# Optimization experiments

Hardware: AMD Instinct MI355X
Metric: run time of the kernel (lower is better)

## Reference

```python
import jax, jax.numpy as jnp
import numpy as np

D, P, MC = 512, 256, 128   # state dim, obs dim, control dim
H, M, T = 32, 64, 1024     # num filters, Hankel/filter length, horizon
GAMMA = 0.9


def setup_inputs() -> dict:
    rng = np.random.default_rng(0)
    # Stable dynamics: scale spectral radius to 0.95
    A = rng.standard_normal((D, D)).astype(np.float32)
    A *= np.float32(0.95 / np.max(np.abs(np.linalg.eigvals(A))))
    B = (rng.standard_normal((D, MC)) / np.sqrt(D)).astype(np.float32)
    C = (rng.standard_normal((P, D)) / np.sqrt(D)).astype(np.float32)
    # SPD cost matrices
    Q_obs = np.eye(P, dtype=np.float32)
    R = (0.1 * np.eye(MC)).astype(np.float32)
    # LQR-like feedback gain (small, applied to y_obs as in the source)
    K = (0.02 * rng.standard_normal((MC, P))).astype(np.float32)
    # Spectral filters from Hankel matrix: Z_ij = gamma^(i+j+2) * 2/((i+j+2)^3-(i+j+2))
    idx = np.arange(M)
    ij = idx[:, None] + idx[None, :] + 2
    Z = (GAMMA ** ij) * 2.0 / (ij ** 3 - ij)
    w, V = np.linalg.eigh(Z)
    sigma = np.abs(w[-H:])
    phi = V[:, -H:]
    sigma_phi = (sigma ** 0.25)[:, None] * phi.T        # [H, M]
    sigma_phi_M = sigma_phi.astype(np.float32)
    # sum over the inner l-loop of sigma_phi_m (the source sums contributions over l)
    s_m = sigma_phi.sum(axis=1).astype(np.float32)       # [H]
    # Learned controller tensor M_il -> [m_control, H, h, p]
    M_tensor = (0.01 * rng.standard_normal((MC, H, H, P))).astype(np.float32)
    x0 = rng.standard_normal(D).astype(np.float32)
    return {
        "A": jnp.asarray(A), "B": jnp.asarray(B), "C": jnp.asarray(C),
        "Q_obs": jnp.asarray(Q_obs), "R": jnp.asarray(R), "K": jnp.asarray(K),
        "M_tensor": jnp.asarray(M_tensor),
        "sigma_phi_M": jnp.asarray(sigma_phi_M), "s_m": jnp.asarray(s_m),
        "x0": jnp.asarray(x0),
    }


def reference(A, B, C, Q_obs, R, K, M_tensor, sigma_phi_M, s_m, x0):
    h, m = sigma_phi_M.shape          # filters, history window
    mc = B.shape[1]
    p = C.shape[0]

    # CAB[i] = C @ A^i @ B for i = 0..h  (Markov parameters for y_nat)
    def pow_step(Ap, _):
        return Ap @ A, C @ (Ap @ B)
    _, CAB = jax.lax.scan(pow_step, jnp.eye(A.shape[0], dtype=A.dtype), None, length=h + 1)  # [h+1, p, mc]

    # Pre-contract M_tensor with the inner filter weights (sum over j/l):
    # u_pert[c] = sum_{i,k,p'} M2[c,i,p'] * sigma_phi_M[i,k] * y_nat_{t-k}[p']
    M2 = jnp.einsum('cijq,j->ciq', M_tensor, s_m)  # [mc, h, p]

    def step(carry, _):
        x, u_buf, y_buf = carry            # x:[d], u_buf:[h+1,mc] newest-first, y_buf:[m,p] newest-first
        y_obs = C @ x                      # [p]
        # natural observation: strip effect of past controls
        y_nat = y_obs - jnp.einsum('ipc,ic->p', CAB, u_buf)
        y_buf = jnp.concatenate([y_nat[None, :], y_buf[:-1]], axis=0)
        # spectral projection of y_nat history, then contract with learned tensor
        y_proj = sigma_phi_M @ y_buf       # [h, p]
        u_pert = jnp.einsum('ciq,iq->c', M2, y_proj)  # [mc]
        u = -(K @ y_obs) + u_pert
        cost = y_obs @ (Q_obs @ y_obs) + u @ (R @ u)
        u_buf = jnp.concatenate([u[None, :], u_buf[:-1]], axis=0)
        x = A @ x + B @ u
        return (x, u_buf, y_buf), cost

    init = (x0,
            jnp.zeros((h + 1, mc), dtype=x0.dtype),
            jnp.zeros((m, p), dtype=x0.dtype))
    _, costs = jax.lax.scan(step, init, None, length=T)
    return costs  # [T] per-step losses
```

## Files before the change

### kernel.cpp

```cpp
#include <hip/hip_runtime.h>

#define TPB 256
#define NWG 160
#define MAXJ 48

__device__ __forceinline__ void cst(float* p, float v) {
  __hip_atomic_store(p, v, __ATOMIC_RELAXED, __HIP_MEMORY_SCOPE_AGENT);
}
__device__ __forceinline__ void cstu(unsigned* p, unsigned v) {
  __hip_atomic_store(p, v, __ATOMIC_RELAXED, __HIP_MEMORY_SCOPE_AGENT);
}
__device__ __forceinline__ float cld(const float* p) {
  return __hip_atomic_load(p, __ATOMIC_RELAXED, __HIP_MEMORY_SCOPE_AGENT);
}
__device__ __forceinline__ float2 cld2(const float* p) {
  unsigned long long u = __hip_atomic_load(
      reinterpret_cast<const unsigned long long*>(p), __ATOMIC_RELAXED,
      __HIP_MEMORY_SCOPE_AGENT);
  float2 v;
  __builtin_memcpy(&v, &u, 8);
  return v;
}

__device__ __forceinline__ void grid_barrier(unsigned* __restrict__ arr,
                                             int bid, int tid, unsigned phase) {
  asm volatile("s_waitcnt vmcnt(0)" ::: "memory");
  __syncthreads();
  if (tid == 0)
    __hip_atomic_store(arr + (bid << 5), phase, __ATOMIC_RELAXED,
                       __HIP_MEMORY_SCOPE_AGENT);
  if (tid < NWG) {
    while (__hip_atomic_load(arr + (tid << 5), __ATOMIC_RELAXED,
                             __HIP_MEMORY_SCOPE_AGENT) < phase)
      __builtin_amdgcn_s_sleep(1);
  }
  __atomic_signal_fence(__ATOMIC_SEQ_CST);
// ... 86 lines not shown
}

__global__ __launch_bounds__(256) void wfir_kernel(const float* __restrict__ M2g,
    const float* __restrict__ Phi, float* __restrict__ W) {
  int idx = blockIdx.x * 256 + threadIdx.x;
  if (idx >= 64 * 32768) return;
  int j = idx >> 15;
  int cq = idx & 32767;
  int c = cq >> 8;
  int q = cq & 255;
  float acc = 0.f;
#pragma unroll
  for (int i = 0; i < 32; ++i)
    acc = fmaf(Phi[(i << 6) | j], M2g[(size_t)(((c << 5) | i) << 8) | q], acc);
  W[idx] = acc;
}

__global__ __launch_bounds__(256) void axpy_acl(const float* __restrict__ A,
    const float* __restrict__ BKC, float* __restrict__ Acl, float* __restrict__ P1) {
  int i = blockIdx.x * 256 + threadIdx.x;
  if (i < 262144) {
    float v = A[i] - BKC[i];
    Acl[i] = v;
    P1[i] = v;
  }
}

__global__ void init_kernel(const float* __restrict__ x0, float* __restrict__ xh,
    float* __restrict__ eh, float* __restrict__ ynh, float* __restrict__ uh0,
    float* __restrict__ dbnd, unsigned* __restrict__ arr) {
  int i = blockIdx.x * 256 + threadIdx.x;
  int stride = gridDim.x * 256;
  for (int k = i; k < 524288; k += stride) cst(xh + k, 0.f);
  for (int k = i; k < 139392; k += stride) cst(eh + k, 0.f);
  for (int k = i; k < 262144; k += stride) cst(ynh + k, 0.f);
  for (int k = i; k < 8192; k += stride) cst(uh0 + k, 0.f);
  for (int k = i; k < NWG * 32; k += stride) cstu(arr + k, 0u);
  if (i < 512) cst(dbnd + i, x0[i]);
}

#define SVIDX(i) ((((i) >> 7) * 132) + ((i) & 127))

__device__ __forceinline__ void stagePad(float* dst, const float* src, int tid) {
  float2 v = cld2(src + (tid << 1));
  int i = tid << 1;
  int a = SVIDX(i);
  dst[a] = v.x;
  dst[a + 1] = v.y;
}

__global__ __launch_bounds__(TPB, 1) void main_kernel(
    const float* __restrict__ B, const float* __restrict__ C,
    const float* __restrict__ x0, const float* __restrict__ Wfir,
    const float* __restrict__ KC, const float* __restrict__ W0C,
    const float* __restrict__ Pp, const float* __restrict__ CApp,
    const float* __restrict__ W0CAp, const float* __restrict__ Rnp,
    const float* __restrict__ AB33p, const float* __restrict__ CAB33p,
    const float* __restrict__ W0CAB33p, const float* __restrict__ A16k,
    float* __restrict__ xh, float* __restrict__ uh0, float* __restrict__ eh,
    float* __restrict__ ynh, float* __restrict__ dbnd,
    unsigned* __restrict__ arr) {
  __shared__ float smA[64 * 256];
  __shared__ float smY[16 * 256];
  __shared__ float smV[528];
  __shared__ float smW[16 * 128];
  __shared__ float redsc[4][16];
  const int bid = blockIdx.x;
  const int tid = threadIdx.x;

  if (bid < 128) {
    for (int i = tid; i < 16384; i += TPB) {
      int j = i >> 8;
      smA[i] = (j >= 1) ? Wfir[(size_t)j * 32768 + bid * 256 + (i & 255)] : 0.f;
    }
  }
  __syncthreads();

  unsigned bcnt = 0;
#pragma unroll 1
  for (int ph = 0; ph <= 64; ++ph) {
    const int T = ph * 16;
    const int Tp = T - 16;

    if (bid < 32) {
      if (ph < 64) {
        const int s = bid >> 1;
        const int half = (bid & 1) << 7;
        stagePad(smV, dbnd + (size_t)ph * 512, tid);
        __syncthreads();
        const float* Mrow = (s == 0) ? C : (CApp + (size_t)(s - 1) * 131072);
        const int row = half + (tid >> 1);
        const int q0 = (tid & 1) * 2;
        const float4* m4 = (const float4*)(Mrow + (size_t)row * 512 + (tid & 1) * 256);
        const float4* v0 = (const float4*)(smV + q0 * 132);
        const float4* v1 = (const float4*)(smV + (q0 + 1) * 132);
        float a0 = 0.f, a1 = 0.f;
#pragma unroll
        for (int it = 0; it < 32; ++it) {
          float4 mm = m4[it], vv = v0[it];
          a0 += mm.x * vv.x + mm.y * vv.y + mm.z * vv.z + mm.w * vv.w;
        }
#pragma unroll
        for (int it = 0; it < 32; ++it) {
          float4 mm = m4[32 + it], vv = v1[it];
          a1 += mm.x * vv.x + mm.y * vv.y + mm.z * vv.z + mm.w * vv.w;
        }
        float a = a0 + a1;
        a += __shfl_down(a, 1);
        if ((tid & 1) == 0) atomicAdd(&ynh[(size_t)(T + s) * 256 + row], a);
        __syncthreads();
      }
    } else if (bid < 48) {
      if (ph < 64) {
        const int g = bid - 32;
        for (int i2 = tid; i2 < 1024; i2 += TPB) {
          float2 v = cld2(uh0 + (size_t)(64 + T - 33) * 128 + 2 * i2);
          smW[2 * i2] = v.x;
          smW[2 * i2 + 1] = v.y;
        }
        __syncthreads();
        const int row = g * 16 + (tid >> 4);
        const int l16 = tid & 15;
        const int qs = l16 * 8;
        float acc[16];
#pragma unroll
        for (int s = 0; s < 16; ++s) acc[s] = 0.f;
#pragma unroll
        for (int m = 0; m < 15; ++m) {
          const float4* cr = (const float4*)(CAB33p + (size_t)m * 32768 + (size_t)row * 128 + qs);
          float4 c0 = cr[0], c1 = cr[1];
#pragma unroll
          for (int s = 0; s < 16; ++s) {
            if (s > m) {
              const float* u = smW + (s - m - 1) * 128 + qs;
              acc[s] += c0.x * u[0] + c0.y * u[1] + c0.z * u[2] + c0.w * u[3] +
                        c1.x * u[4] + c1.y * u[5] + c1.z * u[6] + c1.w * u[7];
            }
          }
        }
#pragma unroll
        for (int s = 0; s < 16; ++s) {
          float v = acc[s];
          v += __shfl_xor(v, 8);
          v += __shfl_xor(v, 4);
          v += __shfl_xor(v, 2);
          v += __shfl_xor(v, 1);
          if (l16 == 0 && s >= 1) atomicAdd(&ynh[(size_t)(T + s) * 256 + row], v);
        }
        __syncthreads();
      }
    } else if (bid < 64) {
      if (ph < 64) {
        const int s = bid - 48;
        stagePad(smV, dbnd + (size_t)ph * 512, tid);
        __syncthreads();
        const float* Mrow = (s == 0) ? W0C : (W0CAp + (size_t)(s - 1) * 65536);
        const int row = tid >> 1;
        const int q0 = (tid & 1) * 2;
        const float4* m4 = (const float4*)(Mrow + (size_t)row * 512 + (tid & 1) * 256);
        const float4* v0 = (const float4*)(smV + q0 * 132);
        const float4* v1 = (const float4*)(smV + (q0 + 1) * 132);
        float a0 = 0.f, a1 = 0.f;
#pragma unroll
        for (int it = 0; it < 32; ++it) {
          float4 mm = m4[it], vv = v0[it];
          a0 += mm.x * vv.x + mm.y * vv.y + mm.z * vv.z + mm.w * vv.w;
        }
#pragma unroll
        for (int it = 0; it < 32; ++it) {
          float4 mm = m4[32 + it], vv = v1[it];
          a1 += mm.x * vv.x + mm.y * vv.y + mm.z * vv.z + mm.w * vv.w;
        }
        float a = a0 + a1;
        a += __shfl_down(a, 1);
        if ((tid & 1) == 0) atomicAdd(&eh[(size_t)(T + s) * 128 + row], a);
        __syncthreads();
      }
    } else if (bid < 72) {
      if (ph < 64) {
        const int g = bid - 64;
        for (int i2 = tid; i2 < 1024; i2 += TPB) {
          float2 v = cld2(uh0 + (size_t)(64 + T - 33) * 128 + 2 * i2);
          smW[2 * i2] = v.x;
          smW[2 * i2 + 1] = v.y;
        }
        __syncthreads();
        const int row = g * 16 + (tid >> 4);
        const int l16 = tid & 15;
        const int qs = l16 * 8;
        float acc[16];
#pragma unroll
        for (int s = 0; s < 16; ++s) acc[s] = 0.f;
#pragma unroll
        for (int m = 0; m < 15; ++m) {
          const float4* cr = (const float4*)(W0CAB33p + (size_t)m * 16384 + (size_t)row * 128 + qs);
          float4 c0 = cr[0], c1 = cr[1];
#pragma unroll
          for (int s = 0; s < 16; ++s) {
            if (s > m) {
              const float* u = smW + (s - m - 1) * 128 + qs;
              acc[s] += c0.x * u[0] + c0.y * u[1] + c0.z * u[2] + c0.w * u[3] +
                        c1.x * u[4] + c1.y * u[5] + c1.z * u[6] + c1.w * u[7];
            }
          }
        }
#pragma unroll
        for (int s = 0; s < 16; ++s) {
          float v = acc[s];
          v += __shfl_xor(v, 8);
          v += __shfl_xor(v, 4);
          v += __shfl_xor(v, 2);
          v += __shfl_xor(v, 1);
          if (l16 == 0 && s >= 1) atomicAdd(&eh[(size_t)(T + s) * 128 + row], v);
        }
        __syncthreads();
      }
    } else if (bid < 88) {
      if (ph < 64) {
        const int g = bid - 72;
        stagePad(smV, dbnd + (size_t)ph * 512, tid);
        for (int i2 = tid; i2 < 1024; i2 += TPB) {
          float2 v = cld2(uh0 + (size_t)(64 + T - 33) * 128 + 2 * i2);
          smW[2 * i2] = v.x;
          smW[2 * i2 + 1] = v.y;
        }
        __syncthreads();
        const int row = g * 32 + (tid >> 3);
        const int l8 = tid & 7;
        float a = 0.f;
        {
          const float4* m4 = (const float4*)(A16k + (size_t)row * 512 + l8 * 64);
          const float4* v4 = (const float4*)(smV + (l8 >> 1) * 132 + (l8 & 1) * 64);
#pragma unroll
          for (int it = 0; it < 16; ++it) {
            float4 mm = m4[it], vv = v4[it];
            a += mm.x * vv.x + mm.y * vv.y + mm.z * vv.z + mm.w * vv.w;
          }
        }
#pragma unroll
        for (int m = 0; m < 16; ++m) {
          const float4* m4 = (const float4*)(AB33p + (size_t)m * 65536 + (size_t)row * 128 + l8 * 16);
          const float4* v4 = (const float4*)(smW + (15 - m) * 128 + l8 * 16);
#pragma unroll
          for (int it = 0; it < 4; ++it) {
            float4 mm = m4[it], vv = v4[it];
            a += mm.x * vv.x + mm.y * vv.y + mm.z * vv.z + mm.w * vv.w;
          }
        }
        a += __shfl_down(a, 4);
        a += __shfl_down(a, 2);
        a += __shfl_down(a, 1);
        if (l8 == 0) cst(&dbnd[(size_t)(ph + 1) * 512 + row], a);
        __syncthreads();
      }
    } else if (bid < 120) {
      if (ph >= 1) {
        const int w = bid - 88;
        const int s = w >> 1;
        const int half = (w & 1) << 8;
        {
          const float* src = (ph == 1) ? x0 : (xh + (size_t)(Tp - 1) * 512);
          stagePad(smV, src, tid);
        }
        __syncthreads();
        const int pslot = (ph == 1) ? s : (s + 1);
        const int row = half + tid;
        if (pslot == 0) {
          atomicAdd(&xh[(size_t)(Tp + s) * 512 + row], smV[SVIDX(row)]);
        } else {
          const float* Mrow = Pp + (size_t)(pslot - 1) * 262144 + (size_t)row * 512;
          const float4* m4 = (const float4*)Mrow;
          float a0 = 0.f, a1 = 0.f, a2 = 0.f, a3 = 0.f;
          const float4* vq0 = (const float4*)(smV);
          const float4* vq1 = (const float4*)(smV + 132);
          const float4* vq2 = (const float4*)(smV + 264);
          const float4* vq3 = (const float4*)(smV + 396);
#pragma unroll
          for (int it = 0; it < 32; ++it) {
            float4 mm = m4[it], vv = vq0[it];
            a0 += mm.x * vv.x + mm.y * vv.y + mm.z * vv.z + mm.w * vv.w;
          }
#pragma unroll
          for (int it = 0; it < 32; ++it) {
            float4 mm = m4[32 + it], vv = vq1[it];
            a1 += mm.x * vv.x + mm.y * vv.y + mm.z * vv.z + mm.w * vv.w;
          }
#pragma unroll
          for (int it = 0; it < 32; ++it) {
            float4 mm = m4[64 + it], vv = vq2[it];
            a2 += mm.x * vv.x + mm.y * vv.y + mm.z * vv.z + mm.w * vv.w;
          }
#pragma unroll
          for (int it = 0; it < 32; ++it) {
            float4 mm = m4[96 + it], vv = vq3[it];
            a3 += mm.x * vv.x + mm.y * vv.y + mm.z * vv.z + mm.w * vv.w;
          }
          atomicAdd(&xh[(size_t)(Tp + s) * 512 + row], (a0 + a1) + (a2 + a3));
        }
        __syncthreads();
      }
    } else {
      if (ph >= 1 && bid < 152) {
        const int g = bid - 120;
        for (int i2 = tid; i2 < 1024; i2 += TPB) {
          int idx = 2 * i2;
          int r = idx >> 7;
          float2 v;
          if (ph == 1 && r == 0) {
            v.x = 0.f;
            v.y = 0.f;
          } else {
            v = cld2(eh + (size_t)(Tp - 1 + r) * 128 + (idx & 127));
          }
          smW[idx] = v.x;
          smW[idx + 1] = v.y;
        }
        __syncthreads();
        const int row = g * 16 + (tid >> 4);
        const int l16 = tid & 15;
        const int qs = l16 * 8;
        float acc[16];
#pragma unroll
        for (int s = 0; s < 16; ++s) acc[s] = 0.f;
#pragma unroll
        for (int i = 0; i < 16; ++i) {
          const float* Rrow = (i == 0) ? (B + (size_t)row * 128 + qs)
                                       : (Rnp + (size_t)(i - 1) * 65536 + (size_t)row * 128 + qs);
          const float4* cr = (const float4*)Rrow;
          float4 c0 = cr[0], c1 = cr[1];
#pragma unroll
          for (int s = 0; s < 16; ++s) {
            if (s >= i) {
              const float* e = smW + (s - i) * 128 + qs;
              acc[s] += c0.x * e[0] + c0.y * e[1] + c0.z * e[2] + c0.w * e[3] +
                        c1.x * e[4] + c1.y * e[5] + c1.z * e[6] + c1.w * e[7];
            }
          }
        }
#pragma unroll
        for (int s = 0; s < 16; ++s) {
          float v = acc[s];
          v += __shfl_xor(v, 8);
          v += __shfl_xor(v, 4);
          v += __shfl_xor(v, 2);
          v += __shfl_xor(v, 1);
          if (l16 == 0) atomicAdd(&xh[(size_t)(Tp + s) * 512 + row], v);
        }
        __syncthreads();
      }
    }

    grid_barrier(arr, bid, tid, ++bcnt);

    if (bid < 128) {
      if (ph < 64) {
        const int c = bid;
        for (int i2 = tid; i2 < 2048; i2 += TPB) {
          float2 v = cld2(ynh + (size_t)T * 256 + 2 * i2);
          smY[2 * i2] = v.x;
          smY[2 * i2 + 1] = v.y;
        }
        __syncthreads();
        const int q = tid;
        float yreg[16];
#pragma unroll
        for (int s = 0; s < 16; ++s) yreg[s] = smY[s * 256 + q];
        const int wv = tid >> 6;
        const int lane = tid & 63;
#pragma unroll
        for (int kt = 0; kt < 5; ++kt) {
          const int r0 = 1 + 16 * kt;
          float wreg[31];
#pragma unroll
          for (int i = 0; i < 31; ++i) {
            const int j = r0 - 15 + i;
            wreg[i] = (j >= 1 && j <= 63) ? smA[j * 256 + q] : 0.f;
          }
          float acc[16];
#pragma unroll
          for (int a = 0; a < 16; ++a) acc[a] = 0.f;
#pragma unroll
          for (int a = 0; a < 16; ++a)
#pragma unroll
            for (int s = 0; s < 16; ++s) acc[a] += wreg[a + 15 - s] * yreg[s];
#pragma unroll
          for (int a = 0; a < 16; ++a) {
            float v = acc[a];
            v += __shfl_xor(v, 32);
            v += __shfl_xor(v, 16);
            v += __shfl_xor(v, 8);
            v += __shfl_xor(v, 4);
            v += __shfl_xor(v, 2);
            v += __shfl_xor(v, 1);
            if (lane == 0) redsc[wv][a] = v;
          }
          __syncthreads();
          if (tid < 16) {
            float sum = redsc[0][tid] + redsc[1][tid] + redsc[2][tid] + redsc[3][tid];
            atomicAdd(&eh[(size_t)(T + r0 + tid) * 128 + c], sum);
          }
          __syncthreads();
        }
      }
    } else {
      if (ph >= 1) {
        const int g = bid - 128;
        const int s = g >> 1;
        const int ch = (g & 1) * 64;
        const int t = Tp + s;
        stagePad(smV, xh + (size_t)t * 512, tid);
        __syncthreads();
        const int row = ch + (tid >> 2);
        const int q0 = tid & 3;
        const float4* m4 = (const float4*)(KC + (size_t)row * 512 + q0 * 128);
        const float4* v4 = (const float4*)(smV + q0 * 132);
        float a = 0.f;
#pragma unroll
        for (int it = 0; it < 32; ++it) {
          float4 mm = m4[it], vv = v4[it];
          a += mm.x * vv.x + mm.y * vv.y + mm.z * vv.z + mm.w * vv.w;
        }
        a += __shfl_down(a, 2);
        a += __shfl_down(a, 1);
        if ((tid & 3) == 0) {
          float u = cld(&eh[(size_t)t * 128 + row]) - a;
          cst(&uh0[(size_t)(64 + t) * 128 + row], u);
        }
        __syncthreads();
      }
    }

    grid_barrier(arr, bid, tid, ++bcnt);
  }
}

__global__ __launch_bounds__(256) void cost_kernel(const float* __restrict__ C,
    const float* __restrict__ Q, const float* __restrict__ R,
    const float* __restrict__ xh, const float* __restrict__ uh0,
    float* __restrict__ out) {
  __shared__ float xs[512];
  __shared__ float ys[256];
  __shared__ float us[128];
  __shared__ float redw[4];
  const int t = blockIdx.x;
  const int tid = threadIdx.x;
  {
    float2 v = cld2(xh + (size_t)t * 512 + 2 * tid);
    xs[2 * tid] = v.x;
    xs[2 * tid + 1] = v.y;
  }
  if (tid < 64) {
    float2 v = cld2(uh0 + (size_t)(64 + t) * 128 + 2 * tid);
    us[2 * tid] = v.x;
    us[2 * tid + 1] = v.y;
  }
  __syncthreads();
  {
    const float4* m4 = (const float4*)(C + (size_t)tid * 512);
    const float4* v4 = (const float4*)xs;
    float a = 0.f;
    for (int it = 0; it < 128; ++it) {
      float4 mm = m4[it], vv = v4[it];
      a += mm.x * vv.x + mm.y * vv.y + mm.z * vv.z + mm.w * vv.w;
    }
    ys[tid] = a;
// ... 11 lines not shown
    float ru = 0.f;
    for (int k = 0; k < 128; ++k) ru = fmaf(Rr[k], us[k], ru);
    acc += ru * us[tid];
  }
  float v = acc;
  v += __shfl_xor(v, 32);
  v += __shfl_xor(v, 16);
  v += __shfl_xor(v, 8);
  v += __shfl_xor(v, 4);
  v += __shfl_xor(v, 2);
  v += __shfl_xor(v, 1);
  if ((tid & 63) == 0) redw[tid >> 6] = v;
  __syncthreads();
  if (tid == 0) out[t] = redw[0] + redw[1] + redw[2] + redw[3];
}

extern "C" void kernel_launch(void* const* d_in, const int* in_sizes, int n_in,
                              void* d_out, int out_size, void* d_ws, size_t ws_size,
                              hipStream_t stream) {
  (void)in_sizes; (void)n_in; (void)out_size; (void)ws_size;
  const float* A = (const float*)d_in[0];
  const float* B = (const float*)d_in[1];
  const float* C = (const float*)d_in[2];
  const float* Q = (const float*)d_in[3];
  const float* R = (const float*)d_in[4];
  const float* Km = (const float*)d_in[5];
  const float* MT = (const float*)d_in[6];
  const float* Phi = (const float*)d_in[7];
  const float* sm = (const float*)d_in[8];
  const float* x0 = (const float*)d_in[9];

  float* ws = (float*)d_ws;
  const int oWfir = 0;
  const int oPp = 2097152;
  const int oCApp = 6291456;
  const int oW0CAp = 8388608;
  const int oRnp = 9437184;
  const int oAB33 = 10485760;
  const int oCAB33 = 11599872;
  const int oW0CAB33 = 12156928;
  const int oA16 = 12435456;
  const int oKC = 12697600;
  const int oW0C = 12763136;
  const int oAcl = 12828672;
  const int oM2 = 13090816;
  const int oA2 = oM2, oA4 = oM2 + 262144, oA8 = oM2 + 524288, oA32 = oM2 + 786432;
  const int oApB = 14139392;
  const int oxh = 15187968;
  const int ouh0 = 15712256;
  const int oeh = 15851520;
  const int oynh = 15990912;
  const int odbnd = 16253056;
  const int oarr = 16286336;
  const int oBKC = oAB33;

  float* xh = ws + oxh;
  float* uh0 = ws + ouh0;
  float* eh = ws + oeh;
  float* ynh = ws + oynh;
  float* dbnd = ws + odbnd;
  unsigned* arr = (unsigned*)(ws + oarr);

  JobBatch jb;
  jb.n = 0;
  jb.start[0] = 0;
  auto J = [&](int xs_, int xo, int ys_, int yo, int zo, int M, int N, int K) {
    int i = jb.n++;
    jb.xsel[i] = xs_; jb.xoff[i] = xo; jb.ysel[i] = ys_; jb.yoff[i] = yo;
    jb.zoff[i] = zo; jb.M[i] = M; jb.N[i] = N; jb.K[i] = K;
    jb.start[i + 1] = jb.start[i] + (M >> 6) * (N >> 6);
  };
  auto L = [&]() {
    multi_gemm<<<dim3(jb.start[jb.n]), dim3(256), 0, stream>>>(jb, A, B, C, Km, ws);
    jb.n = 0;
    jb.start[0] = 0;
  };

  m2_kernel<<<dim3(4096), dim3(256), 0, stream>>>(MT, sm, ws + oM2);
  wfir_kernel<<<dim3(8192), dim3(256), 0, stream>>>(ws + oM2, Phi, ws + oWfir);

  J(4, 0, 3, 0, oKC, 128, 512, 256);
  J(1, 0, 1, 0, oA2, 512, 512, 512);
  J(1, 0, 2, 0, oApB, 512, 128, 512);
  J(3, 0, 1, 0, oCApp, 256, 512, 512);
  L();
  J(2, 0, 0, oKC, oBKC, 512, 512, 128);
  J(0, oA2, 0, oA2, oA4, 512, 512, 512);
  J(0, oCApp, 1, 0, oCApp + 131072, 256, 512, 512);
  J(1, 0, 0, oApB, oApB + 65536, 512, 128, 512);
  J(0, oWfir, 3, 0, oW0C, 128, 512, 256);
  L();
  axpy_acl<<<dim3(1024), dim3(256), 0, stream>>>(A, ws + oBKC, ws + oAcl, ws + oPp);
  J(0, oA4, 0, oA4, oA8, 512, 512, 512);
  J(0, oPp, 0, oPp, oPp + 262144, 512, 512, 512);
  J(0, oCApp, 0, oA2, oCApp + 2 * 131072, 256, 512, 512);
  J(0, oCApp + 131072, 0, oA2, oCApp + 3 * 131072, 256, 512, 512);
  J(0, oW0C, 1, 0, oW0CAp, 128, 512, 512);
  J(0, oW0C, 0, oA2, oW0CAp + 65536, 128, 512, 512);
  J(0, oA2, 0, oApB, oApB + 2 * 65536, 512, 128, 512);
  J(0, oA2, 0, oApB + 65536, oApB + 3 * 65536, 512, 128, 512);
  L();
  J(0, oA8, 0, oA8, oA16, 512, 512, 512);
  J(0, oPp + 262144, 0, oPp, oPp + 2 * 262144, 512, 512, 512);
  J(0, oPp + 262144, 0, oPp + 262144, oPp + 3 * 262144, 512, 512, 512);
  for (int i = 1; i <= 4; ++i)
    J(0, oCApp + (i - 1) * 131072, 0, oA4, oCApp + (i + 3) * 131072, 256, 512, 512);
  for (int i = 1; i <= 2; ++i)
    J(0, oW0CAp + (i - 1) * 65536, 0, oA2, oW0CAp + (i + 1) * 65536, 128, 512, 512);
  for (int i = 1; i <= 4; ++i)
    J(0, oA4, 0, oApB + (i - 1) * 65536, oApB + (i + 3) * 65536, 512, 128, 512);
  L();
  J(0, oA16, 0, oA16, oA32, 512, 512, 512);
  for (int i = 1; i <= 4; ++i)
    J(0, oPp + 3 * 262144, 0, oPp + (i - 1) * 262144, oPp + (i + 3) * 262144, 512, 512, 512);
  for (int i = 1; i <= 8; ++i)
    J(0, oCApp + (i - 1) * 131072, 0, oA8, oCApp + (i + 7) * 131072, 256, 512, 512);
  for (int i = 1; i <= 4; ++i)
    J(0, oW0CAp + (i - 1) * 65536, 0, oA4, oW0CAp + (i + 3) * 65536, 128, 512, 512);
  for (int i = 1; i <= 8; ++i)
    J(0, oA8, 0, oApB + (i - 1) * 65536, oApB + (i + 7) * 65536, 512, 128, 512);
  for (int i = 1; i <= 4; ++i)
    J(0, oPp + (i - 1) * 262144, 2, 0, oRnp + (i - 1) * 65536, 512, 128, 512);
  L();
  for (int i = 1; i <= 8; ++i)
    J(0, oPp + 7 * 262144, 0, oPp + (i - 1) * 262144, oPp + (i + 7) * 262144, 512, 512, 512);
  for (int i = 1; i <= 8; ++i)
    J(0, oW0CAp + (i - 1) * 65536, 0, oA8, oW0CAp + (i + 7) * 65536, 128, 512, 512);
  for (int m = 0; m <= 15; ++m)
    J(0, oA32, 0, oApB + m * 65536, oAB33 + m * 65536, 512, 128, 512);
  for (int i = 5; i <= 8; ++i)
    J(0, oPp + (i - 1) * 262144, 2, 0, oRnp + (i - 1) * 65536, 512, 128, 512);
  L();
  for (int m = 0; m <= 14; ++m)
    J(3, 0, 0, oAB33 + m * 65536, oCAB33 + m * 32768, 256, 128, 512);
  for (int m = 0; m <= 14; ++m)
    J(0, oW0C, 0, oAB33 + m * 65536, oW0CAB33 + m * 16384, 128, 128, 512);
  for (int i = 9; i <= 15; ++i)
    J(0, oPp + (i - 1) * 262144, 2, 0, oRnp + (i - 1) * 65536, 512, 128, 512);
  L();

  init_kernel<<<dim3(2048), dim3(256), 0, stream>>>(x0, xh, eh, ynh, uh0, dbnd, arr);

  main_kernel<<<dim3(NWG), dim3(TPB), 0, stream>>>(
      B, C, x0, ws + oWfir, ws + oKC, ws + oW0C, ws + oPp, ws + oCApp,
      ws + oW0CAp, ws + oRnp, ws + oAB33, ws + oCAB33, ws + oW0CAB33,
      ws + oA16, xh, uh0, eh, ynh, dbnd, arr);

  cost_kernel<<<dim3(1024), dim3(256), 0, stream>>>(C, Q, R, xh, uh0,
                                                    (float*)d_out);
}
```

Before: 3.504 ms.

## Restructure persistent kernel to 8-step blocks with one barrier per phase and more workgroups

The persistent main kernel moves from 16-step blocks with two grid barriers per phase to 8-step blocks (131 phases) with a single grid barrier each. Stages become a software pipeline: y, e, u and x updates for different step blocks run concurrently on separate workgroup groups, and the workgroup count goes from 160 to 214. The host precomputes fewer matrix powers (up to A^8 instead of A^16), which shrinks precompute and the matrix streams read each phase. The cost is more phases and more barriers overall, plus a deeper pipeline whose index offsets must line up exactly.

```diff
diff --git a/kernel.cpp b/kernel.cpp
--- a/kernel.cpp
+++ b/kernel.cpp
@@ -1,7 +1,7 @@
 #include <hip/hip_runtime.h>
 
 #define TPB 256
-#define NWG 160
+#define NWG 214
 #define MAXJ 48
 
 __device__ __forceinline__ void cst(float* p, float v) {
@@ -154,38 +154,29 @@
   int i = blockIdx.x * 256 + threadIdx.x;
   int stride = gridDim.x * 256;
   for (int k = i; k < 524288; k += stride) cst(xh + k, 0.f);
-  for (int k = i; k < 139392; k += stride) cst(eh + k, 0.f);
+  for (int k = i; k < 139264; k += stride) cst(eh + k, 0.f);
   for (int k = i; k < 262144; k += stride) cst(ynh + k, 0.f);
   for (int k = i; k < 8192; k += stride) cst(uh0 + k, 0.f);
   for (int k = i; k < NWG * 32; k += stride) cstu(arr + k, 0u);
   if (i < 512) cst(dbnd + i, x0[i]);
 }
 
-#define SVIDX(i) ((((i) >> 7) * 132) + ((i) & 127))
-
-__device__ __forceinline__ void stagePad(float* dst, const float* src, int tid) {
-  float2 v = cld2(src + (tid << 1));
-  int i = tid << 1;
-  int a = SVIDX(i);
-  dst[a] = v.x;
-  dst[a + 1] = v.y;
-}
-
 __global__ __launch_bounds__(TPB, 1) void main_kernel(
     const float* __restrict__ B, const float* __restrict__ C,
     const float* __restrict__ x0, const float* __restrict__ Wfir,
     const float* __restrict__ KC, const float* __restrict__ W0C,
-    const float* __restrict__ Pp, const float* __restrict__ CApp,
+    const float* __restrict__ Pp, const float* __restrict__ CAp,
     const float* __restrict__ W0CAp, const float* __restrict__ Rnp,
     const float* __restrict__ AB33p, const float* __restrict__ CAB33p,
-    const float* __restrict__ W0CAB33p, const float* __restrict__ A16k,
+    const float* __restrict__ W0CAB33p, const float* __restrict__ A8k,
     float* __restrict__ xh, float* __restrict__ uh0, float* __restrict__ eh,
     float* __restrict__ ynh, float* __restrict__ dbnd,
     unsigned* __restrict__ arr) {
   __shared__ float smA[64 * 256];
-  __shared__ float smY[16 * 256];
-  __shared__ float smV[528];
-  __shared__ float smW[16 * 128];
+  __shared__ float smY[8 * 256];
+  __shared__ float smV[512];
+  __shared__ float smW[8 * 128];
+  __shared__ float smVx[8 * 516];
   __shared__ float redsc[4][16];
   const int bid = blockIdx.x;
   const int tid = threadIdx.x;
@@ -198,304 +189,33 @@
   }
   __syncthreads();
 
-  unsigned bcnt = 0;
 #pragma unroll 1
-  for (int ph = 0; ph <= 64; ++ph) {
-    const int T = ph * 16;
-    const int Tp = T - 16;
-
-    if (bid < 32) {
-      if (ph < 64) {
-        const int s = bid >> 1;
-        const int half = (bid & 1) << 7;
-        stagePad(smV, dbnd + (size_t)ph * 512, tid);
-        __syncthreads();
-        const float* Mrow = (s == 0) ? C : (CApp + (size_t)(s - 1) * 131072);
-        const int row = half + (tid >> 1);
-        const int q0 = (tid & 1) * 2;
-        const float4* m4 = (const float4*)(Mrow + (size_t)row * 512 + (tid & 1) * 256);
-        const float4* v0 = (const float4*)(smV + q0 * 132);
-        const float4* v1 = (const float4*)(smV + (q0 + 1) * 132);
-        float a0 = 0.f, a1 = 0.f;
-#pragma unroll
-        for (int it = 0; it < 32; ++it) {
-          float4 mm = m4[it], vv = v0[it];
-          a0 += mm.x * vv.x + mm.y * vv.y + mm.z * vv.z + mm.w * vv.w;
-        }
-#pragma unroll
-        for (int it = 0; it < 32; ++it) {
-          float4 mm = m4[32 + it], vv = v1[it];
-          a1 += mm.x * vv.x + mm.y * vv.y + mm.z * vv.z + mm.w * vv.w;
-        }
-        float a = a0 + a1;
-        a += __shfl_down(a, 1);
-        if ((tid & 1) == 0) atomicAdd(&ynh[(size_t)(T + s) * 256 + row], a);
-        __syncthreads();
-      }
-    } else if (bid < 48) {
-      if (ph < 64) {
-        const int g = bid - 32;
+  for (int ph = 0; ph <= 130; ++ph) {
+    const int T = ph * 8;
+
+    if (bid < 128) {
+      if (ph >= 1 && ph < 129) {
+        const int Ty = T - 8;
+        const int c = bid;
         for (int i2 = tid; i2 < 1024; i2 += TPB) {
-          float2 v = cld2(uh0 + (size_t)(64 + T - 33) * 128 + 2 * i2);
-          smW[2 * i2] = v.x;
-          smW[2 * i2 + 1] = v.y;
-        }
-        __syncthreads();
-        const int row = g * 16 + (tid >> 4);
-        const int l16 = tid & 15;
-        const int qs = l16 * 8;
-        float acc[16];
-#pragma unroll
-        for (int s = 0; s < 16; ++s) acc[s] = 0.f;
-#pragma unroll
-        for (int m = 0; m < 15; ++m) {
-          const float4* cr = (const float4*)(CAB33p + (size_t)m * 32768 + (size_t)row * 128 + qs);
-          float4 c0 = cr[0], c1 = cr[1];
-#pragma unroll
-          for (int s = 0; s < 16; ++s) {
-            if (s > m) {
-              const float* u = smW + (s - m - 1) * 128 + qs;
-              acc[s] += c0.x * u[0] + c0.y * u[1] + c0.z * u[2] + c0.w * u[3] +
-                        c1.x * u[4] + c1.y * u[5] + c1.z * u[6] + c1.w * u[7];
-            }
-          }
-        }
-#pragma unroll
-        for (int s = 0; s < 16; ++s) {
-          float v = acc[s];
-          v += __shfl_xor(v, 8);
-          v += __shfl_xor(v, 4);
-          v += __shfl_xor(v, 2);
-          v += __shfl_xor(v, 1);
-          if (l16 == 0 && s >= 1) atomicAdd(&ynh[(size_t)(T + s) * 256 + row], v);
-        }
-        __syncthreads();
-      }
-    } else if (bid < 64) {
-      if (ph < 64) {
-        const int s = bid - 48;
-        stagePad(smV, dbnd + (size_t)ph * 512, tid);
-        __syncthreads();
-        const float* Mrow = (s == 0) ? W0C : (W0CAp + (size_t)(s - 1) * 65536);
-        const int row = tid >> 1;
-        const int q0 = (tid & 1) * 2;
-        const float4* m4 = (const float4*)(Mrow + (size_t)row * 512 + (tid & 1) * 256);
-        const float4* v0 = (const float4*)(smV + q0 * 132);
-        const float4* v1 = (const float4*)(smV + (q0 + 1) * 132);
-        float a0 = 0.f, a1 = 0.f;
-#pragma unroll
-        for (int it = 0; it < 32; ++it) {
-          float4 mm = m4[it], vv = v0[it];
-          a0 += mm.x * vv.x + mm.y * vv.y + mm.z * vv.z + mm.w * vv.w;
-        }
-#pragma unroll
-        for (int it = 0; it < 32; ++it) {
-          float4 mm = m4[32 + it], vv = v1[it];
-          a1 += mm.x * vv.x + mm.y * vv.y + mm.z * vv.z + mm.w * vv.w;
-        }
-        float a = a0 + a1;
-        a += __shfl_down(a, 1);
-        if ((tid & 1) == 0) atomicAdd(&eh[(size_t)(T + s) * 128 + row], a);
-        __syncthreads();
-      }
-    } else if (bid < 72) {
-      if (ph < 64) {
-        const int g = bid - 64;
-        for (int i2 = tid; i2 < 1024; i2 += TPB) {
-          float2 v = cld2(uh0 + (size_t)(64 + T - 33) * 128 + 2 * i2);
-          smW[2 * i2] = v.x;
-          smW[2 * i2 + 1] = v.y;
-        }
-        __syncthreads();
-        const int row = g * 16 + (tid >> 4);
-        const int l16 = tid & 15;
-        const int qs = l16 * 8;
-        float acc[16];
-#pragma unroll
-        for (int s = 0; s < 16; ++s) acc[s] = 0.f;
-#pragma unroll
-        for (int m = 0; m < 15; ++m) {
-          const float4* cr = (const float4*)(W0CAB33p + (size_t)m * 16384 + (size_t)row * 128 + qs);
-          float4 c0 = cr[0], c1 = cr[1];
-#pragma unroll
-          for (int s = 0; s < 16; ++s) {
-            if (s > m) {
-              const float* u = smW + (s - m - 1) * 128 + qs;
-              acc[s] += c0.x * u[0] + c0.y * u[1] + c0.z * u[2] + c0.w * u[3] +
-                        c1.x * u[4] + c1.y * u[5] + c1.z * u[6] + c1.w * u[7];
-            }
-          }
-        }
-#pragma unroll
-        for (int s = 0; s < 16; ++s) {
-          float v = acc[s];
-          v += __shfl_xor(v, 8);
-          v += __shfl_xor(v, 4);
-          v += __shfl_xor(v, 2);
-          v += __shfl_xor(v, 1);
-          if (l16 == 0 && s >= 1) atomicAdd(&eh[(size_t)(T + s) * 128 + row], v);
-        }
-        __syncthreads();
-      }
-    } else if (bid < 88) {
-      if (ph < 64) {
-        const int g = bid - 72;
-        stagePad(smV, dbnd + (size_t)ph * 512, tid);
-        for (int i2 = tid; i2 < 1024; i2 += TPB) {
-          float2 v = cld2(uh0 + (size_t)(64 + T - 33) * 128 + 2 * i2);
-          smW[2 * i2] = v.x;
-          smW[2 * i2 + 1] = v.y;
-        }
-        __syncthreads();
-        const int row = g * 32 + (tid >> 3);
-        const int l8 = tid & 7;
-        float a = 0.f;
-        {
-          const float4* m4 = (const float4*)(A16k + (size_t)row * 512 + l8 * 64);
-          const float4* v4 = (const float4*)(smV + (l8 >> 1) * 132 + (l8 & 1) * 64);
-#pragma unroll
-          for (int it = 0; it < 16; ++it) {
-            float4 mm = m4[it], vv = v4[it];
-            a += mm.x * vv.x + mm.y * vv.y + mm.z * vv.z + mm.w * vv.w;
-          }
-        }
-#pragma unroll
-        for (int m = 0; m < 16; ++m) {
-          const float4* m4 = (const float4*)(AB33p + (size_t)m * 65536 + (size_t)row * 128 + l8 * 16);
-          const float4* v4 = (const float4*)(smW + (15 - m) * 128 + l8 * 16);
-#pragma unroll
-          for (int it = 0; it < 4; ++it) {
-            float4 mm = m4[it], vv = v4[it];
-            a += mm.x * vv.x + mm.y * vv.y + mm.z * vv.z + mm.w * vv.w;
-          }
-        }
-        a += __shfl_down(a, 4);
-        a += __shfl_down(a, 2);
-        a += __shfl_down(a, 1);
-        if (l8 == 0) cst(&dbnd[(size_t)(ph + 1) * 512 + row], a);
-        __syncthreads();
-      }
-    } else if (bid < 120) {
-      if (ph >= 1) {
-        const int w = bid - 88;
-        const int s = w >> 1;
-        const int half = (w & 1) << 8;
-        {
-          const float* src = (ph == 1) ? x0 : (xh + (size_t)(Tp - 1) * 512);
-          stagePad(smV, src, tid);
-        }
-        __syncthreads();
-        const int pslot = (ph == 1) ? s : (s + 1);
-        const int row = half + tid;
-        if (pslot == 0) {
-          atomicAdd(&xh[(size_t)(Tp + s) * 512 + row], smV[SVIDX(row)]);
-        } else {
-          const float* Mrow = Pp + (size_t)(pslot - 1) * 262144 + (size_t)row * 512;
-          const float4* m4 = (const float4*)Mrow;
-          float a0 = 0.f, a1 = 0.f, a2 = 0.f, a3 = 0.f;
-          const float4* vq0 = (const float4*)(smV);
-          const float4* vq1 = (const float4*)(smV + 132);
-          const float4* vq2 = (const float4*)(smV + 264);
-          const float4* vq3 = (const float4*)(smV + 396);
-#pragma unroll
-          for (int it = 0; it < 32; ++it) {
-            float4 mm = m4[it], vv = vq0[it];
-            a0 += mm.x * vv.x + mm.y * vv.y + mm.z * vv.z + mm.w * vv.w;
-          }
-#pragma unroll
-          for (int it = 0; it < 32; ++it) {
-            float4 mm = m4[32 + it], vv = vq1[it];
-            a1 += mm.x * vv.x + mm.y * vv.y + mm.z * vv.z + mm.w * vv.w;
-          }
-#pragma unroll
-          for (int it = 0; it < 32; ++it) {
-            float4 mm = m4[64 + it], vv = vq2[it];
-            a2 += mm.x * vv.x + mm.y * vv.y + mm.z * vv.z + mm.w * vv.w;
-          }
-#pragma unroll
-          for (int it = 0; it < 32; ++it) {
-            float4 mm = m4[96 + it], vv = vq3[it];
-            a3 += mm.x * vv.x + mm.y * vv.y + mm.z * vv.z + mm.w * vv.w;
-          }
-          atomicAdd(&xh[(size_t)(Tp + s) * 512 + row], (a0 + a1) + (a2 + a3));
-        }
-        __syncthreads();
-      }
-    } else {
-      if (ph >= 1 && bid < 152) {
-        const int g = bid - 120;
-        for (int i2 = tid; i2 < 1024; i2 += TPB) {
-          int idx = 2 * i2;
-          int r = idx >> 7;
-          float2 v;
-          if (ph == 1 && r == 0) {
-            v.x = 0.f;
-            v.y = 0.f;
-          } else {
-            v = cld2(eh + (size_t)(Tp - 1 + r) * 128 + (idx & 127));
-          }
-          smW[idx] = v.x;
-          smW[idx + 1] = v.y;
-        }
-        __syncthreads();
-        const int row = g * 16 + (tid >> 4);
-        const int l16 = tid & 15;
-        const int qs = l16 * 8;
-        float acc[16];
-#pragma unroll
-        for (int s = 0; s < 16; ++s) acc[s] = 0.f;
-#pragma unroll
-        for (int i = 0; i < 16; ++i) {
-          const float* Rrow = (i == 0) ? (B + (size_t)row * 128 + qs)
-                                       : (Rnp + (size_t)(i - 1) * 65536 + (size_t)row * 128 + qs);
-          const float4* cr = (const float4*)Rrow;
-          float4 c0 = cr[0], c1 = cr[1];
-#pragma unroll
-          for (int s = 0; s < 16; ++s) {
-            if (s >= i) {
-              const float* e = smW + (s - i) * 128 + qs;
-              acc[s] += c0.x * e[0] + c0.y * e[1] + c0.z * e[2] + c0.w * e[3] +
-                        c1.x * e[4] + c1.y * e[5] + c1.z * e[6] + c1.w * e[7];
-            }
-          }
-        }
-#pragma unroll
-        for (int s = 0; s < 16; ++s) {
-          float v = acc[s];
-          v += __shfl_xor(v, 8);
-          v += __shfl_xor(v, 4);
-          v += __shfl_xor(v, 2);
-          v += __shfl_xor(v, 1);
-          if (l16 == 0) atomicAdd(&xh[(size_t)(Tp + s) * 512 + row], v);
-        }
-        __syncthreads();
-      }
-    }
-
-    grid_barrier(arr, bid, tid, ++bcnt);
-
-    if (bid < 128) {
-      if (ph < 64) {
-        const int c = bid;
-        for (int i2 = tid; i2 < 2048; i2 += TPB) {
-          float2 v = cld2(ynh + (size_t)T * 256 + 2 * i2);
+          float2 v = cld2(ynh + (size_t)Ty * 256 + 2 * i2);
           smY[2 * i2] = v.x;
           smY[2 * i2 + 1] = v.y;
         }
         __syncthreads();
         const int q = tid;
-        float yreg[16];
-#pragma unroll
-        for (int s = 0; s < 16; ++s) yreg[s] = smY[s * 256 + q];
+        float yreg[8];
+#pragma unroll
+        for (int s = 0; s < 8; ++s) yreg[s] = smY[s * 256 + q];
         const int wv = tid >> 6;
         const int lane = tid & 63;
 #pragma unroll
         for (int kt = 0; kt < 5; ++kt) {
           const int r0 = 1 + 16 * kt;
-          float wreg[31];
-#pragma unroll
-          for (int i = 0; i < 31; ++i) {
-            const int j = r0 - 15 + i;
+          float wreg[23];
+#pragma unroll
+          for (int i = 0; i < 23; ++i) {
+            const int j = r0 - 7 + i;
             wreg[i] = (j >= 1 && j <= 63) ? smA[j * 256 + q] : 0.f;
           }
           float acc[16];
@@ -504,7 +224,7 @@
 #pragma unroll
           for (int a = 0; a < 16; ++a)
 #pragma unroll
-            for (int s = 0; s < 16; ++s) acc[a] += wreg[a + 15 - s] * yreg[s];
+            for (int s = 0; s < 8; ++s) acc[a] += wreg[a + 7 - s] * yreg[s];
 #pragma unroll
           for (int a = 0; a < 16; ++a) {
             float v = acc[a];
@@ -518,41 +238,255 @@
           }
           __syncthreads();
           if (tid < 16) {
-            float sum = redsc[0][tid] + redsc[1][tid] + redsc[2][tid] + redsc[3][tid];
-            atomicAdd(&eh[(size_t)(T + r0 + tid) * 128 + c], sum);
+            const int r = r0 + tid;
+            if (r <= 70) {
+              float sum = redsc[0][tid] + redsc[1][tid] + redsc[2][tid] + redsc[3][tid];
+              atomicAdd(&eh[(size_t)(Ty + r) * 128 + c], sum);
+            }
           }
           __syncthreads();
         }
       }
-    } else {
-      if (ph >= 1) {
-        const int g = bid - 128;
-        const int s = g >> 1;
-        const int ch = (g & 1) * 64;
-        const int t = Tp + s;
-        stagePad(smV, xh + (size_t)t * 512, tid);
-        __syncthreads();
-        const int row = ch + (tid >> 2);
-        const int q0 = tid & 3;
-        const float4* m4 = (const float4*)(KC + (size_t)row * 512 + q0 * 128);
-        const float4* v4 = (const float4*)(smV + q0 * 132);
+    } else if (bid < 144) {
+      if (ph < 128) {
+        const int r = bid - 128;
+        const int s = r >> 1;
+        const int half = (r & 1) << 7;
+        {
+          float2 v = cld2(dbnd + (size_t)ph * 512 + 2 * tid);
+          smV[2 * tid] = v.x;
+          smV[2 * tid + 1] = v.y;
+        }
+        __syncthreads();
+        const float* Mrow = (s == 0) ? C : (CAp + (size_t)(s - 1) * 131072);
+        const int row = half + (tid >> 1);
+        const int seg = tid & 1;
+        const float4* m4 = (const float4*)(Mrow + (size_t)row * 512 + seg * 256);
+        const float4* v4 = (const float4*)(smV + seg * 256);
         float a = 0.f;
 #pragma unroll
-        for (int it = 0; it < 32; ++it) {
+        for (int it = 0; it < 64; ++it) {
           float4 mm = m4[it], vv = v4[it];
           a += mm.x * vv.x + mm.y * vv.y + mm.z * vv.z + mm.w * vv.w;
         }
+        a += __shfl_down(a, 1);
+        if (seg == 0) atomicAdd(&ynh[(size_t)(T + s) * 256 + row], a);
+        __syncthreads();
+      }
+    } else if (bid < 151) {
+      if (ph < 128) {
+        const int m = bid - 144;
+        for (int i2 = tid; i2 < 512; i2 += TPB) {
+          float2 v = cld2(uh0 + (size_t)(64 + T - 33) * 128 + 2 * i2);
+          smW[2 * i2] = v.x;
+          smW[2 * i2 + 1] = v.y;
+        }
+        __syncthreads();
+        const int row = tid;
+        const float4* m4 = (const float4*)(CAB33p + (size_t)m * 32768 + (size_t)row * 128);
+        for (int s = m + 1; s < 8; ++s) {
+          const float4* u4 = (const float4*)(smW + (s - m - 1) * 128);
+          float a = 0.f;
+#pragma unroll
+          for (int it = 0; it < 32; ++it) {
+            float4 mm = m4[it], vv = u4[it];
+            a += mm.x * vv.x + mm.y * vv.y + mm.z * vv.z + mm.w * vv.w;
+          }
+          atomicAdd(&ynh[(size_t)(T + s) * 256 + row], a);
+        }
+        __syncthreads();
+      }
+    } else if (bid < 159) {
+      if (ph < 128) {
+        const int s = bid - 151;
+        {
+          float2 v = cld2(dbnd + (size_t)ph * 512 + 2 * tid);
+          smV[2 * tid] = v.x;
+          smV[2 * tid + 1] = v.y;
+        }
+        __syncthreads();
+        const float* Mrow = (s == 0) ? W0C : (W0CAp + (size_t)(s - 1) * 65536);
+        const int row = tid >> 1;
+        const int seg = tid & 1;
+        const float4* m4 = (const float4*)(Mrow + (size_t)row * 512 + seg * 256);
+        const float4* v4 = (const float4*)(smV + seg * 256);
+        float a = 0.f;
+#pragma unroll
+        for (int it = 0; it < 64; ++it) {
+          float4 mm = m4[it], vv = v4[it];
+          a += mm.x * vv.x + mm.y * vv.y + mm.z * vv.z + mm.w * vv.w;
+        }
+        a += __shfl_down(a, 1);
+        if (seg == 0) atomicAdd(&eh[(size_t)(T + s) * 128 + row], a);
+        __syncthreads();
+      }
+    } else if (bid < 166) {
+      if (ph < 128) {
+        const int m = bid - 159;
+        for (int i2 = tid; i2 < 512; i2 += TPB) {
+          float2 v = cld2(uh0 + (size_t)(64 + T - 33) * 128 + 2 * i2);
+          smW[2 * i2] = v.x;
+          smW[2 * i2 + 1] = v.y;
+        }
+        __syncthreads();
+        const int row = tid >> 1;
+        const int seg = tid & 1;
+        const float4* m4 = (const float4*)(W0CAB33p + (size_t)m * 16384 + (size_t)row * 128 + seg * 64);
+        for (int s = m + 1; s < 8; ++s) {
+          const float4* u4 = (const float4*)(smW + (s - m - 1) * 128 + seg * 64);
+          float a = 0.f;
+#pragma unroll
+          for (int it = 0; it < 16; ++it) {
+            float4 mm = m4[it], vv = u4[it];
+            a += mm.x * vv.x + mm.y * vv.y + mm.z * vv.z + mm.w * vv.w;
+          }
+          a += __shfl_down(a, 1);
+          if (seg == 0) atomicAdd(&eh[(size_t)(T + s) * 128 + row], a);
+        }
+        __syncthreads();
+      }
+    } else if (bid < 174) {
+      if (ph < 127) {
+        const int g = bid - 166;
+        {
+          float2 v = cld2(dbnd + (size_t)ph * 512 + 2 * tid);
+          smV[2 * tid] = v.x;
+          smV[2 * tid + 1] = v.y;
+        }
+        for (int i2 = tid; i2 < 512; i2 += TPB) {
+          float2 v = cld2(uh0 + (size_t)(64 + T - 33) * 128 + 2 * i2);
+          smW[2 * i2] = v.x;
+          smW[2 * i2 + 1] = v.y;
+        }
+        __syncthreads();
+        const int row = g * 64 + (tid >> 2);
+        const int l4 = tid & 3;
+        float a = 0.f;
+        {
+          const float4* m4 = (const float4*)(A8k + (size_t)row * 512 + l4 * 128);
+          const float4* v4 = (const float4*)(smV + l4 * 128);
+#pragma unroll
+          for (int it = 0; it < 32; ++it) {
+            float4 mm = m4[it], vv = v4[it];
+            a += mm.x * vv.x + mm.y * vv.y + mm.z * vv.z + mm.w * vv.w;
+          }
+        }
+#pragma unroll
+        for (int m = 0; m < 8; ++m) {
+          const float4* m4 = (const float4*)(AB33p + (size_t)m * 65536 + (size_t)row * 128 + l4 * 32);
+          const float4* v4 = (const float4*)(smW + (7 - m) * 128 + l4 * 32);
+#pragma unroll
+          for (int it = 0; it < 8; ++it) {
+            float4 mm = m4[it], vv = v4[it];
+            a += mm.x * vv.x + mm.y * vv.y + mm.z * vv.z + mm.w * vv.w;
+          }
+        }
         a += __shfl_down(a, 2);
         a += __shfl_down(a, 1);
-        if ((tid & 3) == 0) {
-          float u = cld(&eh[(size_t)t * 128 + row]) - a;
-          cst(&uh0[(size_t)(64 + t) * 128 + row], u);
+        if (l4 == 0) cst(&dbnd[(size_t)(ph + 1) * 512 + row], a);
+        __syncthreads();
+      }
+    } else if (bid < 190) {
+      if (ph >= 2 && ph < 130) {
+        const int Tq = T - 16;
+        const int r = bid - 174;
+        const int s = r >> 1;
+        const int half = (r & 1) << 8;
+        {
+          const float* src = (ph == 2) ? x0 : (xh + (size_t)(Tq - 1) * 512);
+          float2 v = cld2(src + 2 * tid);
+          smV[2 * tid] = v.x;
+          smV[2 * tid + 1] = v.y;
+        }
+        __syncthreads();
+        const int pslot = (ph == 2) ? s : (s + 1);
+        const int row = half + tid;
+        if (pslot == 0) {
+          atomicAdd(&xh[(size_t)Tq * 512 + row], smV[row]);
+        } else {
+          const float4* m4 = (const float4*)(Pp + (size_t)(pslot - 1) * 262144 + (size_t)row * 512);
+          const float4* v4 = (const float4*)smV;
+          float a = 0.f;
+#pragma unroll 8
+          for (int it = 0; it < 128; ++it) {
+            float4 mm = m4[it], vv = v4[it];
+            a += mm.x * vv.x + mm.y * vv.y + mm.z * vv.z + mm.w * vv.w;
+          }
+          atomicAdd(&xh[(size_t)(Tq + s) * 512 + row], a);
+        }
+        __syncthreads();
+      }
+    } else if (bid < 206) {
+      if (ph >= 2 && ph < 130) {
+        const int Tq = T - 16;
+        const int r = bid - 190;
+        const int i = r >> 1;
+        const int half = (r & 1) << 8;
+        for (int i2 = tid; i2 < 512; i2 += TPB) {
+          int idx = 2 * i2;
+          float2 v;
+          if (ph == 2 && idx < 128) {
+            v.x = 0.f;
+            v.y = 0.f;
+          } else {
+            v = cld2(eh + (size_t)(Tq - 1) * 128 + idx);
+          }
+          smW[idx] = v.x;
+          smW[idx + 1] = v.y;
+        }
+        __syncthreads();
+        const int row = half + tid;
+        const float* Rrow = (i == 0) ? (B + (size_t)row * 128)
+                                     : (Rnp + (size_t)(i - 1) * 65536 + (size_t)row * 128);
+        const float4* m4 = (const float4*)Rrow;
+        for (int s = i; s < 8; ++s) {
+          const float4* e4 = (const float4*)(smW + (s - i) * 128);
+          float a = 0.f;
+#pragma unroll
+          for (int it = 0; it < 32; ++it) {
+            float4 mm = m4[it], vv = e4[it];
+            a += mm.x * vv.x + mm.y * vv.y + mm.z * vv.z + mm.w * vv.w;
+          }
+          atomicAdd(&xh[(size_t)(Tq + s) * 512 + row], a);
+        }
+        __syncthreads();
+      }
+    } else {
+      if (ph >= 3 && ph < 131) {
+        const int Tu = T - 24;
+        const int g = bid - 206;
+        for (int i2 = tid; i2 < 2048; i2 += TPB) {
+          int idx = 2 * i2;
+          int rr = idx >> 9;
+          int cc = idx & 511;
+          float2 v = cld2(xh + (size_t)(Tu + rr) * 512 + cc);
+          smVx[rr * 516 + cc] = v.x;
+          smVx[rr * 516 + cc + 1] = v.y;
+        }
+        __syncthreads();
+        const int o = tid >> 1;
+        const int par = tid & 1;
+        const int s = o >> 4;
+        const int lr = o & 15;
+        const int row = g * 16 + lr;
+        const float4* m4 = (const float4*)(KC + (size_t)row * 512 + par * 256);
+        const float4* v4 = (const float4*)(smVx + s * 516 + par * 256);
+        float a = 0.f;
+#pragma unroll
+        for (int it = 0; it < 64; ++it) {
+          float4 mm = m4[it], vv = v4[it];
+          a += mm.x * vv.x + mm.y * vv.y + mm.z * vv.z + mm.w * vv.w;
+        }
+        a += __shfl_down(a, 1);
+        if (par == 0) {
+          float u = cld(&eh[(size_t)(Tu + s) * 128 + row]) - a;
+          cst(&uh0[(size_t)(64 + Tu + s) * 128 + row], u);
         }
         __syncthreads();
       }
     }
 
-    grid_barrier(arr, bid, tid, ++bcnt);
+    grid_barrier(arr, bid, tid, (unsigned)(ph + 1));
   }
 }
 
@@ -630,27 +564,30 @@
 
   float* ws = (float*)d_ws;
   const int oWfir = 0;
-  const int oPp = 2097152;
-  const int oCApp = 6291456;
-  const int oW0CAp = 8388608;
-  const int oRnp = 9437184;
-  const int oAB33 = 10485760;
-  const int oCAB33 = 11599872;
-  const int oW0CAB33 = 12156928;
-  const int oA16 = 12435456;
-  const int oKC = 12697600;
-  const int oW0C = 12763136;
-  const int oAcl = 12828672;
-  const int oM2 = 13090816;
-  const int oA2 = oM2, oA4 = oM2 + 262144, oA8 = oM2 + 524288, oA32 = oM2 + 786432;
-  const int oApB = 14139392;
-  const int oxh = 15187968;
-  const int ouh0 = 15712256;
-  const int oeh = 15851520;
-  const int oynh = 15990912;
-  const int odbnd = 16253056;
-  const int oarr = 16286336;
-  const int oBKC = oAB33;
+  const int oKC = 2097152;
+  const int oW0C = 2162688;
+  const int oAcl = 2228224;
+  const int oP = 2490368;
+  const int oCA = 4587520;
+  const int oW0CA = 5505024;
+  const int oRn = 5963776;
+  const int oApB = 6422528;
+  const int oAB33 = 6946816;
+  const int oCAB33 = 7471104;
+  const int oW0CAB33 = 7700480;
+  const int oA2 = 7815168;
+  const int oA4 = 8077312;
+  const int oA8 = 8339456;
+  const int oA16 = 8601600;
+  const int oA32 = 8863744;
+  const int oM2 = 9125888;
+  const int oBKC = oM2;
+  const int oxh = 10174464;
+  const int ouh0 = 10698752;
+  const int oeh = 10838016;
+  const int oynh = 10977280;
+  const int odbnd = 11239424;
+  const int oarr = 11306496;
 
   float* xh = ws + oxh;
   float* uh0 = ws + ouh0;
@@ -674,75 +611,66 @@
     jb.start[0] = 0;
   };
 
+  init_kernel<<<dim3(2048), dim3(256), 0, stream>>>(x0, xh, eh, ynh, uh0, dbnd, arr);
   m2_kernel<<<dim3(4096), dim3(256), 0, stream>>>(MT, sm, ws + oM2);
   wfir_kernel<<<dim3(8192), dim3(256), 0, stream>>>(ws + oM2, Phi, ws + oWfir);
 
   J(4, 0, 3, 0, oKC, 128, 512, 256);
   J(1, 0, 1, 0, oA2, 512, 512, 512);
   J(1, 0, 2, 0, oApB, 512, 128, 512);
-  J(3, 0, 1, 0, oCApp, 256, 512, 512);
+  J(3, 0, 1, 0, oCA, 256, 512, 512);
   L();
   J(2, 0, 0, oKC, oBKC, 512, 512, 128);
   J(0, oA2, 0, oA2, oA4, 512, 512, 512);
-  J(0, oCApp, 1, 0, oCApp + 131072, 256, 512, 512);
+  J(0, oCA, 1, 0, oCA + 131072, 256, 512, 512);
   J(1, 0, 0, oApB, oApB + 65536, 512, 128, 512);
   J(0, oWfir, 3, 0, oW0C, 128, 512, 256);
   L();
-  axpy_acl<<<dim3(1024), dim3(256), 0, stream>>>(A, ws + oBKC, ws + oAcl, ws + oPp);
+  axpy_acl<<<dim3(1024), dim3(256), 0, stream>>>(A, ws + oBKC, ws + oAcl, ws + oP);
   J(0, oA4, 0, oA4, oA8, 512, 512, 512);
-  J(0, oPp, 0, oPp, oPp + 262144, 512, 512, 512);
-  J(0, oCApp, 0, oA2, oCApp + 2 * 131072, 256, 512, 512);
-  J(0, oCApp + 131072, 0, oA2, oCApp + 3 * 131072, 256, 512, 512);
-  J(0, oW0C, 1, 0, oW0CAp, 128, 512, 512);
-  J(0, oW0C, 0, oA2, oW0CAp + 65536, 128, 512, 512);
+  J(0, oP, 0, oP, oP + 262144, 512, 512, 512);
+  J(0, oCA, 0, oA2, oCA + 2 * 131072, 256, 512, 512);
+  J(0, oCA + 131072, 0, oA2, oCA + 3 * 131072, 256, 512, 512);
+  J(0, oW0C, 1, 0, oW0CA, 128, 512, 512);
+  J(0, oW0C, 0, oA2, oW0CA + 65536, 128, 512, 512);
   J(0, oA2, 0, oApB, oApB + 2 * 65536, 512, 128, 512);
   J(0, oA2, 0, oApB + 65536, oApB + 3 * 65536, 512, 128, 512);
   L();
   J(0, oA8, 0, oA8, oA16, 512, 512, 512);
-  J(0, oPp + 262144, 0, oPp, oPp + 2 * 262144, 512, 512, 512);
-  J(0, oPp + 262144, 0, oPp + 262144, oPp + 3 * 262144, 512, 512, 512);
-  for (int i = 1; i <= 4; ++i)
-    J(0, oCApp + (i - 1) * 131072, 0, oA4, oCApp + (i + 3) * 131072, 256, 512, 512);
+  J(0, oP, 0, oP + 262144, oP + 2 * 262144, 512, 512, 512);
+  J(0, oP + 262144, 0, oP + 262144, oP + 3 * 262144, 512, 512, 512);
+  for (int i = 1; i <= 3; ++i)
+    J(0, oCA + (i - 1) * 131072, 0, oA4, oCA + (i + 3) * 131072, 256, 512, 512);
   for (int i = 1; i <= 2; ++i)
-    J(0, oW0CAp + (i - 1) * 65536, 0, oA2, oW0CAp + (i + 1) * 65536, 128, 512, 512);
-  for (int i = 1; i <= 4; ++i)
-    J(0, oA4, 0, oApB + (i - 1) * 65536, oApB + (i + 3) * 65536, 512, 128, 512);
+    J(0, oW0CA + (i - 1) * 65536, 0, oA2, oW0CA + (i + 1) * 65536, 128, 512, 512);
+  for (int k = 1; k <= 4; ++k)
+    J(0, oA4, 0, oApB + (k - 1) * 65536, oApB + (k + 3) * 65536, 512, 128, 512);
+  J(0, oP, 2, 0, oRn, 512, 128, 512);
+  J(0, oP + 262144, 2, 0, oRn + 65536, 512, 128, 512);
   L();
   J(0, oA16, 0, oA16, oA32, 512, 512, 512);
   for (int i = 1; i <= 4; ++i)
-    J(0, oPp + 3 * 262144, 0, oPp + (i - 1) * 262144, oPp + (i + 3) * 262144, 512, 512, 512);
-  for (int i = 1; i <= 8; ++i)
-    J(0, oCApp + (i - 1) * 131072, 0, oA8, oCApp + (i + 7) * 131072, 256, 512, 512);
-  for (int i = 1; i <= 4; ++i)
-    J(0, oW0CAp + (i - 1) * 65536, 0, oA4, oW0CAp + (i + 3) * 65536, 128, 512, 512);
-  for (int i = 1; i <= 8; ++i)
-    J(0, oA8, 0, oApB + (i - 1) * 65536, oApB + (i + 7) * 65536, 512, 128, 512);
-  for (int i = 1; i <= 4; ++i)
-    J(0, oPp + (i - 1) * 262144, 2, 0, oRnp + (i - 1) * 65536, 512, 128, 512);
+    J(0, oP + (i - 1) * 262144, 0, oP + 3 * 262144, oP + (i + 3) * 262144, 512, 512, 512);
+  for (int i = 1; i <= 3; ++i)
+    J(0, oW0CA + (i - 1) * 65536, 0, oA4, oW0CA + (i + 3) * 65536, 128, 512, 512);
+  J(0, oP + 2 * 262144, 2, 0, oRn + 2 * 65536, 512, 128, 512);
+  J(0, oP + 3 * 262144, 2, 0, oRn + 3 * 65536, 512, 128, 512);
   L();
-  for (int i = 1; i <= 8; ++i)
-    J(0, oPp + 7 * 262144, 0, oPp + (i - 1) * 262144, oPp + (i + 7) * 262144, 512, 512, 512);
-  for (int i = 1; i <= 8; ++i)
-    J(0, oW0CAp + (i - 1) * 65536, 0, oA8, oW0CAp + (i + 7) * 65536, 128, 512, 512);
-  for (int m = 0; m <= 15; ++m)
+  for (int m = 0; m <= 7; ++m)
     J(0, oA32, 0, oApB + m * 65536, oAB33 + m * 65536, 512, 128, 512);
-  for (int i = 5; i <= 8; ++i)
-    J(0, oPp + (i - 1) * 262144, 2, 0, oRnp + (i - 1) * 65536, 512, 128, 512);
+  for (int i = 5; i <= 7; ++i)
+    J(0, oP + (i - 1) * 262144, 2, 0, oRn + (i - 1) * 65536, 512, 128, 512);
   L();
-  for (int m = 0; m <= 14; ++m)
+  for (int m = 0; m <= 6; ++m)
     J(3, 0, 0, oAB33 + m * 65536, oCAB33 + m * 32768, 256, 128, 512);
-  for (int m = 0; m <= 14; ++m)
+  for (int m = 0; m <= 6; ++m)
     J(0, oW0C, 0, oAB33 + m * 65536, oW0CAB33 + m * 16384, 128, 128, 512);
-  for (int i = 9; i <= 15; ++i)
-    J(0, oPp + (i - 1) * 262144, 2, 0, oRnp + (i - 1) * 65536, 512, 128, 512);
   L();
 
-  init_kernel<<<dim3(2048), dim3(256), 0, stream>>>(x0, xh, eh, ynh, uh0, dbnd, arr);
-
   main_kernel<<<dim3(NWG), dim3(TPB), 0, stream>>>(
-      B, C, x0, ws + oWfir, ws + oKC, ws + oW0C, ws + oPp, ws + oCApp,
-      ws + oW0CAp, ws + oRnp, ws + oAB33, ws + oCAB33, ws + oW0CAB33,
-      ws + oA16, xh, uh0, eh, ynh, dbnd, arr);
+      B, C, x0, ws + oWfir, ws + oKC, ws + oW0C, ws + oP, ws + oCA,
+      ws + oW0CA, ws + oRn, ws + oAB33, ws + oCAB33, ws + oW0CAB33,
+      ws + oA8, xh, uh0, eh, ynh, dbnd, arr);
 
   cost_kernel<<<dim3(1024), dim3(256), 0, stream>>>(C, Q, R, xh, uh0,
                                                     (float*)d_out);
```

New measurement: 3.325 ms. 5.1% less time.
